# Optimization experiments

Hardware: AMD Instinct MI355X
Metric: run time of the kernel (lower is better)

The kernel has to match this reference:

```python
import jax, jax.numpy as jnp
import numpy as np

B, T, D, H, FF = 4, 2048, 1024, 16, 4096
HD = D // H
EPS = 1e-5


def setup_inputs() -> dict:
    key = jax.random.key(0)
    ks = jax.random.split(key, 10)
    s = lambda k, shape, fan: jax.random.normal(k, shape, jnp.float32) * (1.0 / np.sqrt(fan))
    return {
        "x": jax.random.normal(ks[0], (B, T, D), jnp.float32),
        "ln1_g": jnp.ones((D,), jnp.float32),
        "ln1_b": jnp.zeros((D,), jnp.float32),
        "qkv_w": s(ks[1], (D, 3 * D), D),
        "qkv_b": jnp.zeros((3 * D,), jnp.float32),
        "proj_w": s(ks[2], (D, D), D),
        "proj_b": jnp.zeros((D,), jnp.float32),
        "ln2_g": jnp.ones((D,), jnp.float32),
        "ln2_b": jnp.zeros((D,), jnp.float32),
        "ff1_w": s(ks[3], (D, FF), D),
        "ff1_b": jnp.zeros((FF,), jnp.float32),
        "ff2_w": s(ks[4], (FF, D), FF),
        "ff2_b": jnp.zeros((D,), jnp.float32),
    }


def _layernorm(x, g, b):
    mu = jnp.mean(x, axis=-1, keepdims=True)
    var = jnp.mean(jnp.square(x - mu), axis=-1, keepdims=True)
    return (x - mu) * jax.lax.rsqrt(var + EPS) * g + b


def reference(x, ln1_g, ln1_b, qkv_w, qkv_b, proj_w, proj_b,
              ln2_g, ln2_b, ff1_w, ff1_b, ff2_w, ff2_b):
    # --- attention sublayer ---
    h = _layernorm(x, ln1_g, ln1_b)
    qkv = h @ qkv_w + qkv_b                      # [B,T,3D]
    q, k, v = jnp.split(qkv, 3, axis=-1)
    q = q.reshape(B, T, H, HD).transpose(0, 2, 1, 3)  # [B,H,T,hd]
    k = k.reshape(B, T, H, HD).transpose(0, 2, 1, 3)
    v = v.reshape(B, T, H, HD).transpose(0, 2, 1, 3)
    att = jnp.einsum('bhqd,bhkd->bhqk', q, k) / np.sqrt(HD)
    causal = jnp.tril(jnp.ones((T, T), bool))
    att = jnp.where(causal, att, jnp.finfo(att.dtype).min)
    att = jax.nn.softmax(att, axis=-1)
    out = jnp.einsum('bhqk,bhkd->bhqd', att, v)  # [B,H,T,hd]
    out = out.transpose(0, 2, 1, 3).reshape(B, T, D)
    x = x + out @ proj_w + proj_b
    # --- MLP sublayer ---
    h = _layernorm(x, ln2_g, ln2_b)
    h = jax.nn.gelu(h @ ff1_w + ff1_b, approximate=True)
    x = x + h @ ff2_w + ff2_b
    return x
```

## Files before the change

### kernel.cpp

```cpp
#include <hip/hip_runtime.h>

typedef __attribute__((ext_vector_type(4))) float f32x4;
typedef __attribute__((ext_vector_type(8))) short s16x8;
typedef __attribute__((ext_vector_type(4))) unsigned short u16x4;

#define DEV __device__ __forceinline__

DEV unsigned short f2bf(float f) {
  unsigned int u = __float_as_uint(f);
  return (unsigned short)((u + 0x7FFFu + ((u >> 16) & 1u)) >> 16);
}

DEV float exp2_asm(float x) {
  float r; asm("v_exp_f32 %0, %1" : "=v"(r) : "v"(x)); return r;
}
DEV float rcp_asm(float x) {
  float r; asm("v_rcp_f32 %0, %1" : "=v"(r) : "v"(x)); return r;
}

DEV void gload_lds16(const void* g, void* l) {
  __builtin_amdgcn_global_load_lds(
      (const __attribute__((address_space(1))) unsigned int*)g,
      (__attribute__((address_space(3))) unsigned int*)l, 16, 0, 0);
}

__global__ __launch_bounds__(256) void ln_kernel(
    const float* __restrict__ x, const float* __restrict__ gam,
    const float* __restrict__ bet, unsigned short* __restrict__ o)
{
  const int row = blockIdx.x;
  const int tid = threadIdx.x;
  f32x4 v = *(const f32x4*)(x + (size_t)row * 1024 + tid * 4);
  float s = v[0] + v[1] + v[2] + v[3];
  float s2 = v[0]*v[0] + v[1]*v[1] + v[2]*v[2] + v[3]*v[3];
  #pragma unroll
  for (int m = 1; m < 64; m <<= 1) { s += __shfl_xor(s, m); s2 += __shfl_xor(s2, m); }
  __shared__ float ps[4], ps2[4];
  const int wid = tid >> 6, lane = tid & 63;
  if (lane == 0) { ps[wid] = s; ps2[wid] = s2; }
  __syncthreads();
  s = ps[0] + ps[1] + ps[2] + ps[3];
  s2 = ps2[0] + ps2[1] + ps2[2] + ps2[3];
  const float mu = s * (1.0f / 1024.0f);
  const float rstd = rsqrtf(s2 * (1.0f / 1024.0f) - mu * mu + 1e-5f);
  f32x4 g4 = *(const f32x4*)(gam + tid * 4);
  f32x4 b4 = *(const f32x4*)(bet + tid * 4);
  u16x4 ov;
  #pragma unroll
  for (int j = 0; j < 4; j++) ov[j] = f2bf((v[j] - mu) * rstd * g4[j] + b4[j]);
  *(u16x4*)(o + (size_t)row * 1024 + tid * 4) = ov;
}

__global__ __launch_bounds__(256) void transpose_kernel(
    const float* __restrict__ W, unsigned short* __restrict__ WT, int K, int N)
{
  __shared__ float tile[64][65];
  const int n0 = blockIdx.x * 64, k0 = blockIdx.y * 64;
  const int c = threadIdx.x & 63, r0 = threadIdx.x >> 6;
  #pragma unroll
  for (int r = r0; r < 64; r += 4)
    tile[r][c] = W[(size_t)(k0 + r) * N + n0 + c];
  __syncthreads();
  #pragma unroll
  for (int r = r0; r < 64; r += 4)
    WT[(size_t)(n0 + r) * K + k0 + c] = f2bf(tile[c][r]);
}

template <int MODE>
__global__ __launch_bounds__(512) void gemm8_kernel(
    const unsigned short* __restrict__ A, const unsigned short* __restrict__ WT,
    const float* __restrict__ bias, const float* resid, void* outp,
    int M, int N, int K)
{
  __shared__ unsigned short lds[3 * 24576];
  const int tid = threadIdx.x;
  const int lane = tid & 63, wid = tid >> 6;
  const int l15 = lane & 15, l4 = lane >> 4;
  const int wm = wid >> 2, wn = wid & 3;
  const int tiles_n = N >> 8;
  const int cpx = gridDim.x >> 3;
  const int id = (blockIdx.x & 7) * cpx + (blockIdx.x >> 3);
  const int bm = id / tiles_n, bn = id % tiles_n;
  const int NT = K >> 6;

  const int srow = tid >> 3;
  const int scol = ((tid & 7) ^ (srow & 7)) * 8;
  const unsigned short* Asrc = A  + (size_t)(bm * 128 + srow) * K + scol;
  const unsigned short* Bsrc = WT + (size_t)(bn * 256 + srow) * K + scol;
  const size_t j64 = (size_t)64 * K;
  const int dwave = wid * 1024;

#define STAGE(t_, ss_) do { \
    char* base_ = (char*)lds + (ss_) * 49152 + dwave; \
    const unsigned short* sA_ = Asrc + (size_t)(t_) * 64; \
    const unsigned short* sB_ = Bsrc + (size_t)(t_) * 64; \
    gload_lds16(sA_,            base_); \
    gload_lds16(sA_ + j64,      base_ + 8192); \
    gload_lds16(sB_,            base_ + 16384); \
    gload_lds16(sB_ + j64,      base_ + 16384 + 8192); \
    gload_lds16(sB_ + 2 * j64,  base_ + 16384 + 16384); \
    gload_lds16(sB_ + 3 * j64,  base_ + 16384 + 24576); \
  } while (0)

  f32x4 acc[4][4] = {};

  const int arow0 = wm * 64 + l15;
  const int brow0 = wn * 64 + l15;
  const int cswz = l15 & 7;

  STAGE(0, 0);
  STAGE(1, 1);
  asm volatile("s_waitcnt vmcnt(6)" ::: "memory");
  __builtin_amdgcn_s_barrier();

  int cs = 0, ss = 2;
  for (int t = 0; t < NT; ++t) {
    const unsigned short* sa = lds + cs * 24576;
    const unsigned short* sb = sa + 8192;
    s16x8 af[4][2], bf[4][2];
    #pragma unroll
    for (int mf = 0; mf < 4; ++mf)
      #pragma unroll
      for (int ks = 0; ks < 2; ++ks)
        af[mf][ks] = *(const s16x8*)&sa[(arow0 + mf * 16) * 64 + (((ks * 4 + l4) ^ cswz) * 8)];
    #pragma unroll
    for (int nf = 0; nf < 4; ++nf)
      #pragma unroll
      for (int ks = 0; ks < 2; ++ks)
        bf[nf][ks] = *(const s16x8*)&sb[(brow0 + nf * 16) * 64 + (((ks * 4 + l4) ^ cswz) * 8)];
    if (t + 2 < NT) STAGE(t + 2, ss);
    __builtin_amdgcn_s_setprio(1);
    #pragma unroll
    for (int mf = 0; mf < 4; ++mf)
      #pragma unroll
      for (int nf = 0; nf < 4; ++nf)
        #pragma unroll
        for (int ks = 0; ks < 2; ++ks)
          acc[mf][nf] = __builtin_amdgcn_mfma_f32_16x16x32_bf16(
              af[mf][ks], bf[nf][ks], acc[mf][nf], 0, 0, 0);
    __builtin_amdgcn_s_setprio(0);
    if (t + 2 < NT)      { asm volatile("s_waitcnt vmcnt(6)" ::: "memory"); }
    else if (t + 1 < NT) { asm volatile("s_waitcnt vmcnt(0)" ::: "memory"); }
    __builtin_amdgcn_s_barrier();
    cs = (cs == 2) ? 0 : cs + 1;
    ss = (ss == 2) ? 0 : ss + 1;
  }
#undef STAGE

  #pragma unroll
  for (int nf = 0; nf < 4; nf++) {
    const int col = bn * 256 + wn * 64 + nf * 16 + l15;
    const float bv = bias[col];
    const float qs = (MODE == 0 && col < 1024) ? 0.18033688f : 1.0f;
    #pragma unroll
    for (int mf = 0; mf < 4; mf++) {
      #pragma unroll
      for (int r = 0; r < 4; r++) {
        const int row = bm * 128 + wm * 64 + mf * 16 + l4 * 4 + r;
        const size_t off = (size_t)row * N + col;
        float v = acc[mf][nf][r] + bv;
        if (MODE == 1) {
          ((float*)outp)[off] = v + resid[off];
        } else if (MODE == 2) {
          const float u = v + 0.044715f * v * v * v;
          const float e = exp2_asm(-2.3022010f * u);
          ((unsigned short*)outp)[off] = f2bf(v * rcp_asm(1.0f + e));
        } else {
          ((unsigned short*)outp)[off] = f2bf(v * qs);
        }
      }
    }
  }
}

struct AttnState {
  f32x4 o[4];
  float m, l;
};

DEV void attn_tile(const s16x8* qf, const unsigned short* Ks,
                   const unsigned short* Vt, unsigned short* Pw,
                   AttnState& st, int kv0, int qg, int l15, int l4, bool need_mask)
{
  f32x4 sa[4];
  #pragma unroll
  for (int cb = 0; cb < 4; cb++) sa[cb] = (f32x4){0.f, 0.f, 0.f, 0.f};
  __builtin_amdgcn_s_setprio(1);
  #pragma unroll
  for (int ks = 0; ks < 2; ++ks) {
    #pragma unroll
    for (int cb = 0; cb < 4; cb++) {
      const int kvr = cb * 16 + l15;
      s16x8 bk = *(const s16x8*)&Ks[kvr * 64 + ((ks * 32 + l4 * 8) ^ ((kvr & 7) << 3))];
      sa[cb] = __builtin_amdgcn_mfma_f32_16x16x32_bf16(bk, qf[ks], sa[cb], 0, 0, 0);
    }
  }
  __builtin_amdgcn_s_setprio(0);
  if (need_mask) {
    const int thr = qg - kv0 - l4 * 4;
    #pragma unroll
    for (int cb = 0; cb < 4; cb++)
      #pragma unroll
      for (int r = 0; r < 4; r++)
        if (cb * 16 + r > thr) sa[cb][r] = -3.0e38f;
  }
  float mcb[4];
  #pragma unroll
  for (int cb = 0; cb < 4; cb++)
    mcb[cb] = fmaxf(fmaxf(sa[cb][0], sa[cb][1]), fmaxf(sa[cb][2], sa[cb][3]));
  float mx = fmaxf(fmaxf(mcb[0], mcb[1]), fmaxf(mcb[2], mcb[3]));
  mx = fmaxf(mx, __shfl_xor(mx, 16));
  mx = fmaxf(mx, __shfl_xor(mx, 32));
  const bool skip = __all(mx <= st.m + 11.5f);
  const float mnew = skip ? st.m : fmaxf(st.m, mx);
  float rsum = 0.f;
  #pragma unroll
  for (int cb = 0; cb < 4; cb++) {
    u16x4 pw;
    #pragma unroll
    for (int r = 0; r < 4; r++) {
      const float p = exp2_asm(sa[cb][r] - mnew);
      rsum += p;
      pw[r] = (unsigned short)(__float_as_uint(p) >> 16);
    }
    *(u16x4*)&Pw[l15 * 64 + ((cb * 16 + l4 * 4) ^ ((l15 & 7) << 3))] = pw;
  }
  rsum += __shfl_xor(rsum, 16);
  rsum += __shfl_xor(rsum, 32);
  if (skip) {
    st.l += rsum;
  } else {
    const float alpha = exp2_asm(st.m - mnew);
    st.l = st.l * alpha + rsum;
    st.m = mnew;
    #pragma unroll
    for (int r = 0; r < 4; r++) {
      const float ar = __shfl(alpha, l4 * 4 + r);
      #pragma unroll
      for (int cb = 0; cb < 4; cb++) st.o[cb][r] *= ar;
    }
  }
  asm volatile("s_waitcnt lgkmcnt(0)" ::: "memory");
  __builtin_amdgcn_s_setprio(1);
  #pragma unroll
  for (int ks = 0; ks < 2; ++ks) {
    s16x8 pa = *(const s16x8*)&Pw[l15 * 64 + ((ks * 32 + l4 * 8) ^ ((l15 & 7) << 3))];
    #pragma unroll
    for (int cb = 0; cb < 4; cb++) {
      const int d = cb * 16 + l15;
      s16x8 vf = *(const s16x8*)&Vt[d * 64 + ((ks * 32 + l4 * 8) ^ (((d >> 2) & 7) << 3))];
      st.o[cb] = __builtin_amdgcn_mfma_f32_16x16x32_bf16(pa, vf, st.o[cb], 0, 0, 0);
    }
  }
  __builtin_amdgcn_s_setprio(0);
}

DEV void attn_write(unsigned short* orow, const AttnState& st, int l15, int l4) {
  const float invl = rcp_asm(st.l);
  #pragma unroll
  for (int r = 0; r < 4; r++) {
    const float ir = __shfl(invl, l4 * 4 + r);
    #pragma unroll
    for (int cb = 0; cb < 4; cb++)
      orow[(l4 * 4 + r) * 1024 + cb * 16 + l15] = f2bf(st.o[cb][r] * ir);
  }
}

__global__ __launch_bounds__(256) void attn_kernel(
    const unsigned short* __restrict__ qkv, unsigned short* __restrict__ outb)
{
  __shared__ unsigned short Ks[2][64 * 64];
  __shared__ unsigned short Vt[64 * 64];
  __shared__ unsigned short Ps[2][4][16 * 64];
  const int pid = blockIdx.x;
  const int qA = pid, qB = 31 - pid;
  const int bh = blockIdx.y;
  const int b = bh >> 4, h = bh & 15;
  const int tid = threadIdx.x, lane = tid & 63, wid = tid >> 6;
  const int l15 = lane & 15, l4 = lane >> 4;
  const size_t base = (size_t)b * 2048 * 3072 + (size_t)h * 64;
  const unsigned short* Qb = qkv + base;
  const unsigned short* Kb = qkv + base + 1024;
  const unsigned short* Vb = qkv + base + 2048;

  s16x8 qfA[2], qfB[2];
  {
    const unsigned short* qr = Qb + (size_t)(qA * 64 + wid * 16 + l15) * 3072 + l4 * 8;
    qfA[0] = *(const s16x8*)qr;
    qfA[1] = *(const s16x8*)(qr + 32);
    qr = Qb + (size_t)(qB * 64 + wid * 16 + l15) * 3072 + l4 * 8;
    qfB[0] = *(const s16x8*)qr;
    qfB[1] = *(const s16x8*)(qr + 32);
  }

  u16x4 vv[4];
  #pragma unroll
  for (int it = 0; it < 4; ++it) {
    const int cc = tid + 256 * it;
    vv[it] = *(const u16x4*)(Vb + (size_t)(cc >> 4) * 3072 + (cc & 15) * 4);
  }
  #pragma unroll
  for (int s = 0; s < 2; ++s) {
    const int c = s * 256 + tid;
    const int kv = c >> 3;
    const int dsrc = ((c & 7) * 8) ^ ((kv & 7) << 3);
    gload_lds16(Kb + (size_t)kv * 3072 + dsrc, &Ks[0][(size_t)(c & ~63) * 8]);
  }

  AttnState sA, sB;
  #pragma unroll
  for (int cb = 0; cb < 4; cb++) {
    sA.o[cb] = (f32x4){0.f, 0.f, 0.f, 0.f};
    sB.o[cb] = (f32x4){0.f, 0.f, 0.f, 0.f};
  }
  sA.m = -1e30f; sA.l = 0.f; sB.m = -1e30f; sB.l = 0.f;
  const int qgA = qA * 64 + wid * 16 + l15;
  const int qgB = qB * 64 + wid * 16 + l15;

  for (int kvb = 0; kvb <= qB; ++kvb) {
    const int cur = kvb & 1;
    const int kv0 = kvb * 64;
    __builtin_amdgcn_s_barrier();
    asm volatile("s_waitcnt vmcnt(2)" ::: "memory");
    #pragma unroll
    for (int it = 0; it < 4; ++it) {
      const int cc = tid + 256 * it;
      const int vkv = cc >> 4;
      const int vd = (cc & 15) * 4;
      #pragma unroll
      for (int j = 0; j < 4; j++) {
        const int d = vd + j;
        Vt[d * 64 + (vkv ^ (((d >> 2) & 7) << 3))] = vv[it][j];
      }
    }
    if (kvb < qB) {
      #pragma unroll
      for (int it = 0; it < 4; ++it) {
        const int cc = tid + 256 * it;
        vv[it] = *(const u16x4*)(Vb + (size_t)((kvb + 1) * 64 + (cc >> 4)) * 3072 + (cc & 15) * 4);
      }
      asm volatile("s_waitcnt vmcnt(4)" ::: "memory");
    } else {
      asm volatile("s_waitcnt vmcnt(0)" ::: "memory");
    }
    asm volatile("s_waitcnt lgkmcnt(0)" ::: "memory");
    __builtin_amdgcn_s_barrier();
    if (kvb < qB) {
      #pragma unroll
      for (int s = 0; s < 2; ++s) {
        const int c = s * 256 + tid;
        const int kv = c >> 3;
        const int dsrc = ((c & 7) * 8) ^ ((kv & 7) << 3);
        gload_lds16(Kb + (size_t)((kvb + 1) * 64 + kv) * 3072 + dsrc,
                    &Ks[cur ^ 1][(size_t)(c & ~63) * 8]);
      }
    }
    if (kvb <= qA)
      attn_tile(qfA, Ks[cur], Vt, Ps[0][wid], sA, kv0, qgA, l15, l4,
                kv0 + 63 > qA * 64 + wid * 16);
    attn_tile(qfB, Ks[cur], Vt, Ps[1][wid], sB, kv0, qgB, l15, l4,
              kv0 + 63 > qB * 64 + wid * 16);
  }
  attn_write(outb + ((size_t)b * 2048 + qA * 64 + wid * 16) * 1024 + h * 64, sA, l15, l4);
  attn_write(outb + ((size_t)b * 2048 + qB * 64 + wid * 16) * 1024 + h * 64, sB, l15, l4);
}

extern "C" void kernel_launch(void* const* d_in, const int* in_sizes, int n_in,
                              void* d_out, int out_size, void* d_ws, size_t ws_size,
                              hipStream_t stream) {
  const float* x      = (const float*)d_in[0];
  const float* ln1_g  = (const float*)d_in[1];
  const float* ln1_b  = (const float*)d_in[2];
  const float* qkv_w  = (const float*)d_in[3];
  const float* qkv_b  = (const float*)d_in[4];
  const float* proj_w = (const float*)d_in[5];
  const float* proj_b = (const float*)d_in[6];
  const float* ln2_g  = (const float*)d_in[7];
  const float* ln2_b  = (const float*)d_in[8];
  const float* ff1_w  = (const float*)d_in[9];
  const float* ff1_b  = (const float*)d_in[10];
  const float* ff2_w  = (const float*)d_in[11];
  const float* ff2_b  = (const float*)d_in[12];
  float* out = (float*)d_out;

  char* ws = (char*)d_ws;
  size_t off = 0;
  unsigned short* wbuf   = (unsigned short*)(ws + off); off += (size_t)4096 * 1024 * 2;
  unsigned short* hbuf   = (unsigned short*)(ws + off); off += (size_t)8192 * 1024 * 2;
  unsigned short* qkvbuf = (unsigned short*)(ws + off); off += (size_t)8192 * 3072 * 2;
  unsigned short* gbuf   = (unsigned short*)(ws + off);

  ln_kernel<<<8192, 256, 0, stream>>>(x, ln1_g, ln1_b, hbuf);
  transpose_kernel<<<dim3(3072 / 64, 1024 / 64), 256, 0, stream>>>(qkv_w, wbuf, 1024, 3072);
  gemm8_kernel<0><<<dim3(64 * 12), 512, 0, stream>>>(hbuf, wbuf, qkv_b, nullptr, qkvbuf,
                                                     8192, 3072, 1024);
  attn_kernel<<<dim3(16, 64), 256, 0, stream>>>(qkvbuf, hbuf);
  transpose_kernel<<<dim3(1024 / 64, 1024 / 64), 256, 0, stream>>>(proj_w, wbuf, 1024, 1024);
  gemm8_kernel<1><<<dim3(64 * 4), 512, 0, stream>>>(hbuf, wbuf, proj_b, x, out,
                                                    8192, 1024, 1024);
  ln_kernel<<<8192, 256, 0, stream>>>(out, ln2_g, ln2_b, hbuf);
  transpose_kernel<<<dim3(4096 / 64, 1024 / 64), 256, 0, stream>>>(ff1_w, wbuf, 1024, 4096);
  gemm8_kernel<2><<<dim3(64 * 16), 512, 0, stream>>>(hbuf, wbuf, ff1_b, nullptr, gbuf,
                                                     8192, 4096, 1024);
  transpose_kernel<<<dim3(1024 / 64, 4096 / 64), 256, 0, stream>>>(ff2_w, wbuf, 4096, 1024);
  gemm8_kernel<1><<<dim3(64 * 4), 512, 0, stream>>>(gbuf, wbuf, ff2_b, out, out,
                                                    8192, 1024, 4096);
}
```

Baseline: 440.9 us.

## Rewrite attention with 32x32x16 MFMA and register-resident P via permlane swap

Restructures the attention kernel so each wave owns 32 query rows of one tile (two waves per q-block) and uses 32x32x16 bf16 MFMAs for both QK^T and PV. The softmax probabilities are repacked into A-operand layout in registers with v_permlane32_swap instead of a round trip through LDS, and the per-row rescale factors go through a small LDS array. This removes the P staging buffer and the LDS traffic and waits tied to it, and adds a launch-bounds occupancy hint. The cost is that waves working on the short q-block sit idle for more iterations, which can unbalance work inside the block, and register pressure rises from the 16-wide accumulators.

```diff
diff --git a/kernel.cpp b/kernel.cpp
--- a/kernel.cpp
+++ b/kernel.cpp
@@ -1,8 +1,10 @@
 #include <hip/hip_runtime.h>
 
 typedef __attribute__((ext_vector_type(4))) float f32x4;
+typedef __attribute__((ext_vector_type(16))) float f32x16;
 typedef __attribute__((ext_vector_type(8))) short s16x8;
 typedef __attribute__((ext_vector_type(4))) unsigned short u16x4;
+typedef __attribute__((ext_vector_type(4))) unsigned int u32x4;
 
 #define DEV __device__ __forceinline__
 
@@ -16,6 +18,12 @@
 }
 DEV float rcp_asm(float x) {
   float r; asm("v_rcp_f32 %0, %1" : "=v"(r) : "v"(x)); return r;
+}
+DEV unsigned int pk2(float a, float b) {
+  return (__float_as_uint(b) & 0xFFFF0000u) | (__float_as_uint(a) >> 16);
+}
+DEV void pl32swap(unsigned int& x, unsigned int& y) {
+  asm volatile("v_permlane32_swap_b32 %0, %1" : "+v"(x), "+v"(y));
 }
 
 DEV void gload_lds16(const void* g, void* l) {
@@ -173,124 +181,32 @@
   }
 }
 
-struct AttnState {
-  f32x4 o[4];
-  float m, l;
-};
-
-DEV void attn_tile(const s16x8* qf, const unsigned short* Ks,
-                   const unsigned short* Vt, unsigned short* Pw,
-                   AttnState& st, int kv0, int qg, int l15, int l4, bool need_mask)
-{
-  f32x4 sa[4];
-  #pragma unroll
-  for (int cb = 0; cb < 4; cb++) sa[cb] = (f32x4){0.f, 0.f, 0.f, 0.f};
-  __builtin_amdgcn_s_setprio(1);
-  #pragma unroll
-  for (int ks = 0; ks < 2; ++ks) {
-    #pragma unroll
-    for (int cb = 0; cb < 4; cb++) {
-      const int kvr = cb * 16 + l15;
-      s16x8 bk = *(const s16x8*)&Ks[kvr * 64 + ((ks * 32 + l4 * 8) ^ ((kvr & 7) << 3))];
-      sa[cb] = __builtin_amdgcn_mfma_f32_16x16x32_bf16(bk, qf[ks], sa[cb], 0, 0, 0);
-    }
-  }
-  __builtin_amdgcn_s_setprio(0);
-  if (need_mask) {
-    const int thr = qg - kv0 - l4 * 4;
-    #pragma unroll
-    for (int cb = 0; cb < 4; cb++)
-      #pragma unroll
-      for (int r = 0; r < 4; r++)
-        if (cb * 16 + r > thr) sa[cb][r] = -3.0e38f;
-  }
-  float mcb[4];
-  #pragma unroll
-  for (int cb = 0; cb < 4; cb++)
-    mcb[cb] = fmaxf(fmaxf(sa[cb][0], sa[cb][1]), fmaxf(sa[cb][2], sa[cb][3]));
-  float mx = fmaxf(fmaxf(mcb[0], mcb[1]), fmaxf(mcb[2], mcb[3]));
-  mx = fmaxf(mx, __shfl_xor(mx, 16));
-  mx = fmaxf(mx, __shfl_xor(mx, 32));
-  const bool skip = __all(mx <= st.m + 11.5f);
-  const float mnew = skip ? st.m : fmaxf(st.m, mx);
-  float rsum = 0.f;
-  #pragma unroll
-  for (int cb = 0; cb < 4; cb++) {
-    u16x4 pw;
-    #pragma unroll
-    for (int r = 0; r < 4; r++) {
-      const float p = exp2_asm(sa[cb][r] - mnew);
-      rsum += p;
-      pw[r] = (unsigned short)(__float_as_uint(p) >> 16);
-    }
-    *(u16x4*)&Pw[l15 * 64 + ((cb * 16 + l4 * 4) ^ ((l15 & 7) << 3))] = pw;
-  }
-  rsum += __shfl_xor(rsum, 16);
-  rsum += __shfl_xor(rsum, 32);
-  if (skip) {
-    st.l += rsum;
-  } else {
-    const float alpha = exp2_asm(st.m - mnew);
-    st.l = st.l * alpha + rsum;
-    st.m = mnew;
-    #pragma unroll
-    for (int r = 0; r < 4; r++) {
-      const float ar = __shfl(alpha, l4 * 4 + r);
-      #pragma unroll
-      for (int cb = 0; cb < 4; cb++) st.o[cb][r] *= ar;
-    }
-  }
-  asm volatile("s_waitcnt lgkmcnt(0)" ::: "memory");
-  __builtin_amdgcn_s_setprio(1);
-  #pragma unroll
-  for (int ks = 0; ks < 2; ++ks) {
-    s16x8 pa = *(const s16x8*)&Pw[l15 * 64 + ((ks * 32 + l4 * 8) ^ ((l15 & 7) << 3))];
-    #pragma unroll
-    for (int cb = 0; cb < 4; cb++) {
-      const int d = cb * 16 + l15;
-      s16x8 vf = *(const s16x8*)&Vt[d * 64 + ((ks * 32 + l4 * 8) ^ (((d >> 2) & 7) << 3))];
-      st.o[cb] = __builtin_amdgcn_mfma_f32_16x16x32_bf16(pa, vf, st.o[cb], 0, 0, 0);
-    }
-  }
-  __builtin_amdgcn_s_setprio(0);
-}
-
-DEV void attn_write(unsigned short* orow, const AttnState& st, int l15, int l4) {
-  const float invl = rcp_asm(st.l);
-  #pragma unroll
-  for (int r = 0; r < 4; r++) {
-    const float ir = __shfl(invl, l4 * 4 + r);
-    #pragma unroll
-    for (int cb = 0; cb < 4; cb++)
-      orow[(l4 * 4 + r) * 1024 + cb * 16 + l15] = f2bf(st.o[cb][r] * ir);
-  }
-}
-
-__global__ __launch_bounds__(256) void attn_kernel(
+__global__ __launch_bounds__(256, 4) void attn_kernel(
     const unsigned short* __restrict__ qkv, unsigned short* __restrict__ outb)
 {
   __shared__ unsigned short Ks[2][64 * 64];
   __shared__ unsigned short Vt[64 * 64];
-  __shared__ unsigned short Ps[2][4][16 * 64];
+  __shared__ float alf[4][32];
   const int pid = blockIdx.x;
   const int qA = pid, qB = 31 - pid;
   const int bh = blockIdx.y;
   const int b = bh >> 4, h = bh & 15;
   const int tid = threadIdx.x, lane = tid & 63, wid = tid >> 6;
-  const int l15 = lane & 15, l4 = lane >> 4;
+  const int l31 = lane & 31, hi = lane >> 5;
+  const int myq = (wid < 2) ? qA : qB;
+  const int qbase = myq * 64 + (wid & 1) * 32;
   const size_t base = (size_t)b * 2048 * 3072 + (size_t)h * 64;
   const unsigned short* Qb = qkv + base;
   const unsigned short* Kb = qkv + base + 1024;
   const unsigned short* Vb = qkv + base + 2048;
 
-  s16x8 qfA[2], qfB[2];
+  s16x8 qf[4];
   {
-    const unsigned short* qr = Qb + (size_t)(qA * 64 + wid * 16 + l15) * 3072 + l4 * 8;
-    qfA[0] = *(const s16x8*)qr;
-    qfA[1] = *(const s16x8*)(qr + 32);
-    qr = Qb + (size_t)(qB * 64 + wid * 16 + l15) * 3072 + l4 * 8;
-    qfB[0] = *(const s16x8*)qr;
-    qfB[1] = *(const s16x8*)(qr + 32);
+    const unsigned short* qr = Qb + (size_t)(qbase + l31) * 3072 + hi * 8;
+    qf[0] = *(const s16x8*)(qr);
+    qf[1] = *(const s16x8*)(qr + 16);
+    qf[2] = *(const s16x8*)(qr + 32);
+    qf[3] = *(const s16x8*)(qr + 48);
   }
 
   u16x4 vv[4];
@@ -307,15 +223,9 @@
     gload_lds16(Kb + (size_t)kv * 3072 + dsrc, &Ks[0][(size_t)(c & ~63) * 8]);
   }
 
-  AttnState sA, sB;
-  #pragma unroll
-  for (int cb = 0; cb < 4; cb++) {
-    sA.o[cb] = (f32x4){0.f, 0.f, 0.f, 0.f};
-    sB.o[cb] = (f32x4){0.f, 0.f, 0.f, 0.f};
-  }
-  sA.m = -1e30f; sA.l = 0.f; sB.m = -1e30f; sB.l = 0.f;
-  const int qgA = qA * 64 + wid * 16 + l15;
-  const int qgB = qB * 64 + wid * 16 + l15;
+  f32x16 o0 = {0,0,0,0,0,0,0,0,0,0,0,0,0,0,0,0};
+  f32x16 o1 = {0,0,0,0,0,0,0,0,0,0,0,0,0,0,0,0};
+  float m = -1e30f, lsum = 0.f;
 
   for (int kvb = 0; kvb <= qB; ++kvb) {
     const int cur = kvb & 1;
@@ -355,14 +265,101 @@
                     &Ks[cur ^ 1][(size_t)(c & ~63) * 8]);
       }
     }
-    if (kvb <= qA)
-      attn_tile(qfA, Ks[cur], Vt, Ps[0][wid], sA, kv0, qgA, l15, l4,
-                kv0 + 63 > qA * 64 + wid * 16);
-    attn_tile(qfB, Ks[cur], Vt, Ps[1][wid], sB, kv0, qgB, l15, l4,
-              kv0 + 63 > qB * 64 + wid * 16);
-  }
-  attn_write(outb + ((size_t)b * 2048 + qA * 64 + wid * 16) * 1024 + h * 64, sA, l15, l4);
-  attn_write(outb + ((size_t)b * 2048 + qB * 64 + wid * 16) * 1024 + h * 64, sB, l15, l4);
+
+    if (kvb <= myq) {
+      const unsigned short* Kc = Ks[cur];
+      f32x16 s0 = {0,0,0,0,0,0,0,0,0,0,0,0,0,0,0,0};
+      f32x16 s1 = {0,0,0,0,0,0,0,0,0,0,0,0,0,0,0,0};
+      __builtin_amdgcn_s_setprio(1);
+      #pragma unroll
+      for (int c = 0; c < 4; ++c) {
+        const int koff = ((2 * c + hi) ^ (l31 & 7)) * 8;
+        s16x8 k0 = *(const s16x8*)&Kc[l31 * 64 + koff];
+        s16x8 k1 = *(const s16x8*)&Kc[(32 + l31) * 64 + koff];
+        s0 = __builtin_amdgcn_mfma_f32_32x32x16_bf16(k0, qf[c], s0, 0, 0, 0);
+        s1 = __builtin_amdgcn_mfma_f32_32x32x16_bf16(k1, qf[c], s1, 0, 0, 0);
+      }
+      __builtin_amdgcn_s_setprio(0);
+      if (kv0 + 63 > qbase) {
+        const int thr = qbase + l31 - kv0;
+        #pragma unroll
+        for (int r = 0; r < 16; ++r) {
+          const int kvl = (r & 3) + 8 * (r >> 2) + 4 * hi;
+          if (kvl > thr)      s0[r] = -3.0e38f;
+          if (kvl + 32 > thr) s1[r] = -3.0e38f;
+        }
+      }
+      float mx = s0[0];
+      #pragma unroll
+      for (int r = 1; r < 16; ++r) mx = fmaxf(mx, s0[r]);
+      #pragma unroll
+      for (int r = 0; r < 16; ++r) mx = fmaxf(mx, s1[r]);
+      mx = fmaxf(mx, __shfl_xor(mx, 32));
+      const bool skip = __all(mx <= m + 11.5f);
+      const float mnew = skip ? m : fmaxf(m, mx);
+      float rsum = 0.f;
+      #pragma unroll
+      for (int r = 0; r < 16; ++r) { s0[r] = exp2_asm(s0[r] - mnew); rsum += s0[r]; }
+      #pragma unroll
+      for (int r = 0; r < 16; ++r) { s1[r] = exp2_asm(s1[r] - mnew); rsum += s1[r]; }
+      rsum += __shfl_xor(rsum, 32);
+      if (skip) {
+        lsum += rsum;
+      } else {
+        const float alpha = exp2_asm(m - mnew);
+        lsum = lsum * alpha + rsum;
+        m = mnew;
+        alf[wid][l31] = alpha;
+        #pragma unroll
+        for (int r = 0; r < 16; ++r) {
+          const float ar = alf[wid][(r & 3) + 8 * (r >> 2) + 4 * hi];
+          o0[r] *= ar; o1[r] *= ar;
+        }
+      }
+      s16x8 pa[4];
+      #pragma unroll
+      for (int kb = 0; kb < 2; ++kb) {
+        #pragma unroll
+        for (int cc = 0; cc < 2; ++cc) {
+          const int rb = cc * 8;
+          unsigned int X0, Y0, X1, Y1;
+          if (kb == 0) {
+            X0 = pk2(s0[rb + 0], s0[rb + 1]); Y0 = pk2(s0[rb + 4], s0[rb + 5]);
+            X1 = pk2(s0[rb + 2], s0[rb + 3]); Y1 = pk2(s0[rb + 6], s0[rb + 7]);
+          } else {
+            X0 = pk2(s1[rb + 0], s1[rb + 1]); Y0 = pk2(s1[rb + 4], s1[rb + 5]);
+            X1 = pk2(s1[rb + 2], s1[rb + 3]); Y1 = pk2(s1[rb + 6], s1[rb + 7]);
+          }
+          pl32swap(X0, Y0);
+          pl32swap(X1, Y1);
+          u32x4 w = {X0, X1, Y0, Y1};
+          pa[kb * 2 + cc] = __builtin_bit_cast(s16x8, w);
+        }
+      }
+      const int voff = l31 >> 2;
+      __builtin_amdgcn_s_setprio(1);
+      #pragma unroll
+      for (int c = 0; c < 4; ++c) {
+        const int off = ((2 * c + hi) ^ voff) * 8;
+        s16x8 v0 = *(const s16x8*)&Vt[l31 * 64 + off];
+        s16x8 v1 = *(const s16x8*)&Vt[(32 + l31) * 64 + off];
+        o0 = __builtin_amdgcn_mfma_f32_32x32x16_bf16(pa[c], v0, o0, 0, 0, 0);
+        o1 = __builtin_amdgcn_mfma_f32_32x32x16_bf16(pa[c], v1, o1, 0, 0, 0);
+      }
+      __builtin_amdgcn_s_setprio(0);
+    }
+  }
+
+  const float iv = rcp_asm(lsum);
+  alf[wid][l31] = iv;
+  unsigned short* ob = outb + ((size_t)b * 2048 + qbase) * 1024 + h * 64 + l31;
+  #pragma unroll
+  for (int r = 0; r < 16; ++r) {
+    const int ql = (r & 3) + 8 * (r >> 2) + 4 * hi;
+    const float ir = alf[wid][ql];
+    ob[(size_t)ql * 1024]      = f2bf(o0[r] * ir);
+    ob[(size_t)ql * 1024 + 32] = f2bf(o1[r] * ir);
+  }
 }
 
 extern "C" void kernel_launch(void* const* d_in, const int* in_sizes, int n_in,
```

Measured after the change: 455.5 us (median of 2 runs). 1.03x slower.
